# Performance work log

Hardware: AMD Instinct MI355X
Metric: run time of the kernel (lower is better)

Reference implementation:

```python
import jax, jax.numpy as jnp
import numpy as np
from jax import lax

WQ_MAX = 7.0    # int4 narrow symmetric range [-7, 7]
AQ_MAX = 15.0   # uint4 range [0, 15]
BN_EPS = 1e-5


def quant_weight(w):
    # per-output-channel symmetric int4 fake quant (OIHW, channel axis 0)
    s = jnp.max(jnp.abs(w), axis=(1, 2, 3), keepdims=True) / WQ_MAX
    s = jnp.maximum(s, 1e-8)
    return jnp.clip(jnp.round(w / s), -WQ_MAX, WQ_MAX) * s


def quant_relu(x, s):
    # ReLU fused with uint4 fake quant (clip at 0 subsumes ReLU)
    return jnp.clip(jnp.round(x / s), 0.0, AQ_MAX) * s


def conv2d(x, w, stride, pad, groups=1):
    return lax.conv_general_dilated(
        x, w, (stride, stride), [(pad, pad), (pad, pad)],
        feature_group_count=groups,
        dimension_numbers=('NCHW', 'OIHW', 'NCHW'))


def bn(x, g, b, m, v):
    inv = g / jnp.sqrt(v + BN_EPS)
    return x * inv[None, :, None, None] + (b - m * inv)[None, :, None, None]


def qconv_bn_qrelu(x, w, g, b, m, v, s, stride, pad, groups=1):
    x = conv2d(x, quant_weight(w), stride, pad, groups)
    return quant_relu(bn(x, g, b, m, v), s)


def setup_inputs() -> dict:
    key = jax.random.key(0)
    ks = jax.random.split(key, 8)
    d1, d2, oc = 32, 48, 64
    inp = {'x': jax.random.normal(ks[0], (8, 3, 512, 1024), dtype=jnp.float32)}

    def bn_params(c, tag):
        return {f'g{tag}': jnp.ones((c,), jnp.float32),
                f'b{tag}': jnp.zeros((c,), jnp.float32),
                f'm{tag}': jnp.zeros((c,), jnp.float32),
                f'v{tag}': jnp.ones((c,), jnp.float32)}

    inp['w1'] = 0.1 * jax.random.normal(ks[1], (d1, 3, 3, 3), jnp.float32)
    inp.update(bn_params(d1, 1)); inp['s1'] = jnp.float32(0.1)
    inp['wdw1'] = 0.1 * jax.random.normal(ks[2], (d1, 1, 3, 3), jnp.float32)
    inp.update(bn_params(d1, 2)); inp['s2'] = jnp.float32(0.1)
    inp['wpw1'] = 0.1 * jax.random.normal(ks[3], (d2, d1, 1, 1), jnp.float32)
    inp.update(bn_params(d2, 3)); inp['s3'] = jnp.float32(0.1)
    inp['wdw2'] = 0.1 * jax.random.normal(ks[4], (d2, 1, 3, 3), jnp.float32)
    inp.update(bn_params(d2, 4)); inp['s4'] = jnp.float32(0.1)
    inp['wpw2'] = 0.1 * jax.random.normal(ks[5], (oc, d2, 1, 1), jnp.float32)
    inp.update(bn_params(oc, 5)); inp['s5'] = jnp.float32(0.1)
    return inp


def reference(x, w1, g1, b1, m1, v1, s1,
              wdw1, g2, b2, m2, v2, s2,
              wpw1, g3, b3, m3, v3, s3,
              wdw2, g4, b4, m4, v4, s4,
              wpw2, g5, b5, m5, v5, s5):
    # _ConvBNReLU: 3x3 stride 2, padding 0
    x = qconv_bn_qrelu(x, w1, g1, b1, m1, v1, s1, stride=2, pad=0)
    # _DSConv 1: depthwise 3x3 s2 p1 (groups=32) + pointwise 1x1
    x = qconv_bn_qrelu(x, wdw1, g2, b2, m2, v2, s2, stride=2, pad=1, groups=32)
    x = qconv_bn_qrelu(x, wpw1, g3, b3, m3, v3, s3, stride=1, pad=0)
    # _DSConv 2: depthwise 3x3 s2 p1 (groups=48) + pointwise 1x1
    x = qconv_bn_qrelu(x, wdw2, g4, b4, m4, v4, s4, stride=2, pad=1, groups=48)
    x = qconv_bn_qrelu(x, wpw2, g5, b5, m5, v5, s5, stride=1, pad=0)
    return x  # [8, 64, 64, 128]
```

## Files before the change

kernel.cpp:

```cpp
#include <hip/hip_runtime.h>
#include <stdint.h>

#define AQ_MAX 15.0f
#define BN_EPS 1e-5f

__global__ __launch_bounds__(64) void prep_all(
    const float* __restrict__ wA, const float* __restrict__ gA,
    const float* __restrict__ bA, const float* __restrict__ mA,
    const float* __restrict__ vA,
    const float* __restrict__ wB, const float* __restrict__ gB,
    const float* __restrict__ bB, const float* __restrict__ mB,
    const float* __restrict__ vB,
    const float* __restrict__ wC, const float* __restrict__ gC,
    const float* __restrict__ bC, const float* __restrict__ mC,
    const float* __restrict__ vC,
    const float* __restrict__ wD, const float* __restrict__ gD,
    const float* __restrict__ bD, const float* __restrict__ mD,
    const float* __restrict__ vD,
    const float* __restrict__ wE, const float* __restrict__ gE,
    const float* __restrict__ bE, const float* __restrict__ mE,
    const float* __restrict__ vE,
    float* __restrict__ P) {
  int blk = blockIdx.x, t = threadIdx.x;
  const float *w, *g, *b, *m, *v;
  float *wq, *inv, *beta;
  int K, KP, c;
  if (blk < 32) {
    c = blk; w = wA; g = gA; b = bA; m = mA; v = vA; K = 27; KP = 28;
    wq = P + 0; inv = P + 6224; beta = P + 6256;
  } else if (blk < 64) {
    c = blk - 32; w = wB; g = gB; b = bB; m = mB; v = vB; K = 9; KP = 9;
    wq = P + 896; inv = P + 6288; beta = P + 6320;
  } else if (blk < 112) {
    c = blk - 64; w = wC; g = gC; b = bC; m = mC; v = vC; K = 32; KP = 32;
    wq = P + 1184; inv = P + 6352; beta = P + 6400;
  } else if (blk < 160) {
    c = blk - 112; w = wD; g = gD; b = bD; m = mD; v = vD; K = 9; KP = 9;
    wq = P + 2720; inv = P + 6448; beta = P + 6496;
  } else {
    c = blk - 160; w = wE; g = gE; b = bE; m = mE; v = vE; K = 48; KP = 48;
    wq = P + 3152; inv = P + 6544; beta = P + 6608;
  }
  const float* wc = w + (size_t)c * K;
  float a = (t < K) ? fabsf(wc[t]) : 0.0f;
#pragma unroll
  for (int off = 32; off >= 1; off >>= 1) a = fmaxf(a, __shfl_xor(a, off));
  float s = fmaxf(a / 7.0f, 1e-8f);
  if (t < K) {
    float q = rintf(wc[t] / s);
    q = fminf(7.0f, fmaxf(-7.0f, q));
    wq[(size_t)c * KP + t] = q * s;
  } else if (t < KP) {
    wq[(size_t)c * KP + t] = 0.0f;
  }
  if (t == 0) {
    float iv = g[c] / sqrtf(v[c] + BN_EPS);
    inv[c] = iv;
    beta[c] = b[c] - m[c] * iv;
  }
}

__global__ __launch_bounds__(256) void stage1_kernel(
    const float* __restrict__ x, const float* __restrict__ P,
    const float* __restrict__ s1p, uint8_t* __restrict__ out) {
  int tid = blockIdx.x * 256 + threadIdx.x;
  int gx = tid & 255;
  int t2 = tid >> 8;
  int oy = t2 % 255;
  int n = t2 / 255;
  float s1 = *s1p;
  int ix0 = gx * 4, iy = 2 * oy;
  bool tailok = (ix0 + 4) < 1024;
  float r[9][5];
#pragma unroll
  for (int ic = 0; ic < 3; ic++)
#pragma unroll
    for (int kh = 0; kh < 3; kh++) {
      const float* bp = x + (((size_t)(n * 3 + ic)) * 512 + (iy + kh)) * 1024 + ix0;
      float4 f = *(const float4*)bp;
      int s = ic * 3 + kh;
      r[s][0] = f.x; r[s][1] = f.y; r[s][2] = f.z; r[s][3] = f.w;
      r[s][4] = tailok ? bp[4] : 0.0f;
    }
  size_t obase = (((size_t)n * 32) * 255 + oy) * 256 + gx;
#pragma unroll 2
  for (int oc = 0; oc < 32; oc++) {
    const float* wp = P + oc * 28;
    float w[27];
#pragma unroll
    for (int j = 0; j < 27; j++) w[j] = wp[j];
    float a0 = 0.0f, a1 = 0.0f;
#pragma unroll
    for (int s = 0; s < 9; s++) {
#pragma unroll
      for (int kw = 0; kw < 3; kw++) {
        float wv = w[s * 3 + kw];
        a0 = fmaf(r[s][0 + kw], wv, a0);
        a1 = fmaf(r[s][2 + kw], wv, a1);
      }
    }
    float iv = P[6224 + oc], bt = P[6256 + oc];
    float y0 = fmaf(a0, iv, bt), y1 = fmaf(a1, iv, bt);
    uint32_t q0 = (uint32_t)fminf(AQ_MAX, fmaxf(0.0f, rintf(y0 / s1)));
    uint32_t q1 = (uint32_t)fminf(AQ_MAX, fmaxf(0.0f, rintf(y1 / s1)));
    out[obase + (size_t)oc * (255 * 256)] = (uint8_t)(q0 | (q1 << 4));
  }
}

template <int C, int IH, int IWL, int IWP, int OH, int OW, bool NIB>
__global__ __launch_bounds__(256) void dw_kernel(
    const uint8_t* __restrict__ in, const float* __restrict__ wq,
    const float* __restrict__ inv, const float* __restrict__ beta,
    const float* __restrict__ sin_p, const float* __restrict__ sout_p,
    uint8_t* __restrict__ out) {
  constexpr int GX = OW / 4;
  constexpr bool HASPAD = NIB ? (IWL < 2 * IWP) : (IWL < IWP);
  int tid = blockIdx.x * 256 + threadIdx.x;
  int oxg = tid % GX;
  int t2 = tid / GX;
  int oy = t2 % OH;
  int t3 = t2 / OH;
  int c = __builtin_amdgcn_readfirstlane(t3 % C);
  int n = __builtin_amdgcn_readfirstlane(t3 / C);
  float s_in = *sin_p, s_out = *sout_p;
  const float* wc = wq + c * 9;
  float w[9];
#pragma unroll
  for (int j = 0; j < 9; j++) w[j] = wc[j];
  float iv = inv[c], bt = beta[c];
  int c0 = oxg * 8;
  const uint8_t* chan = in + ((size_t)(n * C + c)) * IH * IWP;
  float xr[3][9];
#pragma unroll
  for (int kh = 0; kh < 3; kh++) {
    int iy = 2 * oy + kh - 1;
    if (iy >= 0 && iy < IH) {
      const uint8_t* rp = chan + (size_t)iy * IWP;
      if (NIB) {
        uint32_t u = *(const uint32_t*)(rp + c0 / 2);
        xr[kh][0] = (oxg > 0) ? (float)((rp[c0 / 2 - 1] >> 4) & 15u) : 0.0f;
#pragma unroll
        for (int j = 0; j < 8; j++)
          xr[kh][1 + j] = (float)((u >> (4 * j)) & 15u);
      } else {
        uint2 u = *(const uint2*)(rp + c0);
        xr[kh][0] = (oxg > 0) ? (float)rp[c0 - 1] : 0.0f;
#pragma unroll
        for (int j = 0; j < 4; j++) xr[kh][1 + j] = (float)((u.x >> (8 * j)) & 255u);
#pragma unroll
        for (int j = 0; j < 4; j++) xr[kh][5 + j] = (float)((u.y >> (8 * j)) & 255u);
      }
      if (HASPAD && oxg == GX - 1) xr[kh][8] = 0.0f;
    } else {
#pragma unroll
      for (int j = 0; j < 9; j++) xr[kh][j] = 0.0f;
    }
  }
#pragma unroll
  for (int kh = 0; kh < 3; kh++)
#pragma unroll
    for (int j = 0; j < 9; j++) xr[kh][j] *= s_in;
  float acc[4] = {0, 0, 0, 0};
#pragma unroll
  for (int kh = 0; kh < 3; kh++)
#pragma unroll
    for (int kw = 0; kw < 3; kw++) {
      float wv = w[kh * 3 + kw];
#pragma unroll
      for (int p = 0; p < 4; p++) acc[p] = fmaf(xr[kh][2 * p + kw], wv, acc[p]);
    }
  uint32_t pack = 0;
#pragma unroll
  for (int p = 0; p < 4; p++) {
    float y = fmaf(acc[p], iv, bt);
    float q = fminf(AQ_MAX, fmaxf(0.0f, rintf(y / s_out)));
    pack |= ((uint32_t)q) << (8 * p);
  }
  *(uint32_t*)(out + ((size_t)(n * C + c) * OH + oy) * OW + c0 / 2) = pack;
}

template <int IC, int OC, int CHUNK, int HW, bool FINAL, bool ROT>
__global__ __launch_bounds__(256) void pw_kernel(
    const uint8_t* __restrict__ in, const float* __restrict__ Pw,
    const float* __restrict__ Pinv, const float* __restrict__ Pbeta,
    const float* __restrict__ sin_p, const float* __restrict__ sout_p,
    void* __restrict__ outv) {
  constexpr int NCH = OC / CHUNK;
  int tid = blockIdx.x * 256 + threadIdx.x;
  int px = tid % HW;
  int rest = tid / HW;
  int chunk = __builtin_amdgcn_readfirstlane(rest % NCH);
  int n = __builtin_amdgcn_readfirstlane(rest / NCH);
  float s_in = *sin_p, s_out = *sout_p;
  const uint8_t* ib = in + (size_t)n * IC * HW + px;
  float xa[IC];
#pragma unroll
  for (int ic = 0; ic < IC; ic++)
    xa[ic] = (float)ib[(size_t)ic * HW] * s_in;
  int oc0 = chunk * CHUNK;
  if (ROT) {
    float wcur[IC], wnxt[IC], ivc, btc, ivn, btn;
#pragma unroll
    for (int j = 0; j < IC; j++) wcur[j] = Pw[(size_t)oc0 * IC + j];
    ivc = Pinv[oc0]; btc = Pbeta[oc0];
#pragma unroll
    for (int k = 0; k < CHUNK; k++) {
      int oc = oc0 + k;
      if (k < CHUNK - 1) {
#pragma unroll
        for (int j = 0; j < IC; j++) wnxt[j] = Pw[(size_t)(oc + 1) * IC + j];
        ivn = Pinv[oc + 1]; btn = Pbeta[oc + 1];
      }
      float a0 = 0;
#pragma unroll
      for (int ic = 0; ic < IC; ic++) a0 = fmaf(xa[ic], wcur[ic], a0);
      float y0 = fmaf(a0, ivc, btc);
      float q0 = fminf(AQ_MAX, fmaxf(0.0f, rintf(y0 / s_out)));
      if (FINAL) {
        ((float*)outv)[((size_t)n * OC + oc) * HW + px] = q0 * s_out;
      } else {
        ((uint8_t*)outv)[((size_t)n * OC + oc) * HW + px] = (uint8_t)q0;
      }
      if (k < CHUNK - 1) {
#pragma unroll
        for (int j = 0; j < IC; j++) wcur[j] = wnxt[j];
        ivc = ivn; btc = btn;
      }
    }
  } else {
#pragma unroll 2
    for (int oc = oc0; oc < oc0 + CHUNK; oc++) {
      const float* wp = Pw + (size_t)oc * IC;
      float w[IC];
#pragma unroll
      for (int ic = 0; ic < IC; ic++) w[ic] = wp[ic];
      float a0 = 0;
#pragma unroll
      for (int ic = 0; ic < IC; ic++) a0 = fmaf(xa[ic], w[ic], a0);
      float iv = Pinv[oc], bt = Pbeta[oc];
      float y0 = fmaf(a0, iv, bt);
      float q0 = fminf(AQ_MAX, fmaxf(0.0f, rintf(y0 / s_out)));
      if (FINAL) {
        ((float*)outv)[((size_t)n * OC + oc) * HW + px] = q0 * s_out;
      } else {
        ((uint8_t*)outv)[((size_t)n * OC + oc) * HW + px] = (uint8_t)q0;
      }
    }
  }
}

extern "C" void kernel_launch(void* const* d_in, const int* in_sizes, int n_in,
                              void* d_out, int out_size, void* d_ws, size_t ws_size,
                              hipStream_t stream) {
  const float* x    = (const float*)d_in[0];
  const float* w1   = (const float*)d_in[1];
  const float* g1   = (const float*)d_in[2];
  const float* b1   = (const float*)d_in[3];
  const float* m1   = (const float*)d_in[4];
  const float* v1   = (const float*)d_in[5];
  const float* s1   = (const float*)d_in[6];
  const float* wdw1 = (const float*)d_in[7];
  const float* g2   = (const float*)d_in[8];
  const float* b2   = (const float*)d_in[9];
  const float* m2   = (const float*)d_in[10];
  const float* v2   = (const float*)d_in[11];
  const float* s2   = (const float*)d_in[12];
  const float* wpw1 = (const float*)d_in[13];
  const float* g3   = (const float*)d_in[14];
  const float* b3   = (const float*)d_in[15];
  const float* m3   = (const float*)d_in[16];
  const float* v3   = (const float*)d_in[17];
  const float* s3   = (const float*)d_in[18];
  const float* wdw2 = (const float*)d_in[19];
  const float* g4   = (const float*)d_in[20];
  const float* b4   = (const float*)d_in[21];
  const float* m4   = (const float*)d_in[22];
  const float* v4   = (const float*)d_in[23];
  const float* s4   = (const float*)d_in[24];
  const float* wpw2 = (const float*)d_in[25];
  const float* g5   = (const float*)d_in[26];
  const float* b5   = (const float*)d_in[27];
  const float* m5   = (const float*)d_in[28];
  const float* v5   = (const float*)d_in[29];
  const float* s5   = (const float*)d_in[30];

  float* P = (float*)d_ws;
  float* wq2  = P + 896;
  float* wq3  = P + 1184;
  float* wq4  = P + 2720;
  float* wq5  = P + 3152;
  float* inv2 = P + 6288, *beta2 = P + 6320;
  float* inv3 = P + 6352, *beta3 = P + 6400;
  float* inv4 = P + 6448, *beta4 = P + 6496;
  float* inv5 = P + 6544, *beta5 = P + 6608;

  uint8_t* ws8 = (uint8_t*)d_ws;
  uint8_t* x1 = ws8 + 32768;
  uint8_t* x2 = x1 + 16711680;
  uint8_t* x3 = x2 + 8388608;
  uint8_t* x4 = ws8 + 32768;

  prep_all<<<224, 64, 0, stream>>>(w1, g1, b1, m1, v1,
                                   wdw1, g2, b2, m2, v2,
                                   wpw1, g3, b3, m3, v3,
                                   wdw2, g4, b4, m4, v4,
                                   wpw2, g5, b5, m5, v5, P);

  stage1_kernel<<<2040, 256, 0, stream>>>(x, P, s1, x1);
  dw_kernel<32, 255, 511, 256, 128, 256, true>
      <<<8192, 256, 0, stream>>>(x1, wq2, inv2, beta2, s1, s2, x2);
  pw_kernel<32, 48, 48, 32768, false, true>
      <<<1024, 256, 0, stream>>>(x2, wq3, inv3, beta3, s2, s3, x3);
  dw_kernel<48, 128, 256, 256, 64, 128, false>
      <<<3072, 256, 0, stream>>>(x3, wq4, inv4, beta4, s3, s4, x4);
  pw_kernel<48, 64, 16, 8192, true, false>
      <<<1024, 256, 0, stream>>>(x4, wq5, inv5, beta5, s4, s5, (float*)d_out);
}
```

Before: 113.4 us.

## Fuse pointwise1, depthwise2 and pointwise2 into one tiled shared-memory kernel

Replaces the last three kernels (pw1, dw2, pw2) with a single kernel. Each block handles an 8x8 output tile: it computes the 17x17 pw1 halo region into LDS, then the depthwise stride-2 conv into LDS, then the final pointwise conv straight to global memory. This removes the global round trips of the x3 and x4 intermediates and two kernel launches. In exchange it recomputes the halo overlap of pw1, and the second pass of the halo load leaves most threads idle.

```diff
diff --git a/kernel.cpp b/kernel.cpp
--- a/kernel.cpp
+++ b/kernel.cpp
@@ -179,72 +179,116 @@
   *(uint32_t*)(out + ((size_t)(n * C + c) * OH + oy) * OW + c0 / 2) = pack;
 }
 
-template <int IC, int OC, int CHUNK, int HW, bool FINAL, bool ROT>
-__global__ __launch_bounds__(256) void pw_kernel(
-    const uint8_t* __restrict__ in, const float* __restrict__ Pw,
-    const float* __restrict__ Pinv, const float* __restrict__ Pbeta,
-    const float* __restrict__ sin_p, const float* __restrict__ sout_p,
-    void* __restrict__ outv) {
-  constexpr int NCH = OC / CHUNK;
-  int tid = blockIdx.x * 256 + threadIdx.x;
-  int px = tid % HW;
-  int rest = tid / HW;
-  int chunk = __builtin_amdgcn_readfirstlane(rest % NCH);
-  int n = __builtin_amdgcn_readfirstlane(rest / NCH);
-  float s_in = *sin_p, s_out = *sout_p;
-  const uint8_t* ib = in + (size_t)n * IC * HW + px;
-  float xa[IC];
-#pragma unroll
-  for (int ic = 0; ic < IC; ic++)
-    xa[ic] = (float)ib[(size_t)ic * HW] * s_in;
-  int oc0 = chunk * CHUNK;
-  if (ROT) {
-    float wcur[IC], wnxt[IC], ivc, btc, ivn, btn;
-#pragma unroll
-    for (int j = 0; j < IC; j++) wcur[j] = Pw[(size_t)oc0 * IC + j];
-    ivc = Pinv[oc0]; btc = Pbeta[oc0];
-#pragma unroll
-    for (int k = 0; k < CHUNK; k++) {
-      int oc = oc0 + k;
-      if (k < CHUNK - 1) {
-#pragma unroll
-        for (int j = 0; j < IC; j++) wnxt[j] = Pw[(size_t)(oc + 1) * IC + j];
-        ivn = Pinv[oc + 1]; btn = Pbeta[oc + 1];
+__global__ __launch_bounds__(256) void fuse_tail(
+    const uint8_t* __restrict__ x2,
+    const float* __restrict__ Wpw1, const float* __restrict__ Ipw1,
+    const float* __restrict__ Bpw1,
+    const float* __restrict__ Wdw2, const float* __restrict__ Idw2,
+    const float* __restrict__ Bdw2,
+    const float* __restrict__ Wpw2, const float* __restrict__ Ipw2,
+    const float* __restrict__ Bpw2,
+    const float* __restrict__ s2p, const float* __restrict__ s3p,
+    const float* __restrict__ s4p, const float* __restrict__ s5p,
+    float* __restrict__ out) {
+  __shared__ uint8_t mid3[48 * 17 * 20];
+  __shared__ uint8_t mid4[48 * 8 * 12];
+  int bid = blockIdx.x;
+  int tx = bid & 15;
+  int t2b = bid >> 4;
+  int ty = t2b & 7;
+  int n = t2b >> 3;
+  int y0 = ty * 8, x0 = tx * 8;
+  float s2 = *s2p, s3 = *s3p, s4 = *s4p, s5 = *s5p;
+
+  for (int k = 0; k < 2; k++) {
+    int t = threadIdx.x + k * 256;
+    if (t < 289) {
+      int lr = t / 17, lc = t % 17;
+      int gr = 2 * y0 - 1 + lr, gc = 2 * x0 - 1 + lc;
+      if (gr < 0 || gc < 0) {
+#pragma unroll 4
+        for (int ch = 0; ch < 48; ch++) mid3[ch * 340 + lr * 20 + lc] = 0;
+      } else {
+        const uint8_t* ib = x2 + (size_t)n * 32 * 32768 + (size_t)gr * 256 + gc;
+        float xa[32];
+#pragma unroll
+        for (int ic = 0; ic < 32; ic++)
+          xa[ic] = (float)ib[(size_t)ic * 32768] * s2;
+#pragma unroll 2
+        for (int oc = 0; oc < 48; oc++) {
+          const float* wp = Wpw1 + oc * 32;
+          float w[32];
+#pragma unroll
+          for (int ic = 0; ic < 32; ic++) w[ic] = wp[ic];
+          float a0 = 0;
+#pragma unroll
+          for (int ic = 0; ic < 32; ic++) a0 = fmaf(xa[ic], w[ic], a0);
+          float y = fmaf(a0, Ipw1[oc], Bpw1[oc]);
+          float q = fminf(AQ_MAX, fmaxf(0.0f, rintf(y / s3)));
+          mid3[oc * 340 + lr * 20 + lc] = (uint8_t)q;
+        }
       }
+    }
+  }
+  __syncthreads();
+
+  {
+    int chg = __builtin_amdgcn_readfirstlane(threadIdx.x >> 6);
+    int pxid = threadIdx.x & 63;
+    int ly = pxid >> 3, lx = pxid & 7;
+#pragma unroll 2
+    for (int i = 0; i < 12; i++) {
+      int ch = chg * 12 + i;
+      const float* wc = Wdw2 + ch * 9;
+      float w[9];
+#pragma unroll
+      for (int j = 0; j < 9; j++) w[j] = wc[j];
+      float iv = Idw2[ch], bt = Bdw2[ch];
+      float xr[3][3];
+#pragma unroll
+      for (int kh = 0; kh < 3; kh++)
+#pragma unroll
+        for (int kw = 0; kw < 3; kw++)
+          xr[kh][kw] = (float)mid3[ch * 340 + (2 * ly + kh) * 20 + (2 * lx + kw)];
+#pragma unroll
+      for (int kh = 0; kh < 3; kh++)
+#pragma unroll
+        for (int kw = 0; kw < 3; kw++) xr[kh][kw] *= s3;
+      float acc = 0;
+#pragma unroll
+      for (int kh = 0; kh < 3; kh++)
+#pragma unroll
+        for (int kw = 0; kw < 3; kw++)
+          acc = fmaf(xr[kh][kw], w[kh * 3 + kw], acc);
+      float y = fmaf(acc, iv, bt);
+      float q = fminf(AQ_MAX, fmaxf(0.0f, rintf(y / s4)));
+      mid4[ch * 96 + ly * 12 + lx] = (uint8_t)q;
+    }
+  }
+  __syncthreads();
+
+  {
+    int ocg = __builtin_amdgcn_readfirstlane(threadIdx.x >> 6);
+    int pxid = threadIdx.x & 63;
+    int ly = pxid >> 3, lx = pxid & 7;
+    float xa[48];
+#pragma unroll
+    for (int ic = 0; ic < 48; ic++)
+      xa[ic] = (float)mid4[ic * 96 + ly * 12 + lx] * s4;
+    size_t ob = ((size_t)n * 64) * (64 * 128) + (size_t)(y0 + ly) * 128 + (x0 + lx);
+#pragma unroll 2
+    for (int k = 0; k < 16; k++) {
+      int oc = ocg * 16 + k;
+      const float* wp = Wpw2 + oc * 48;
+      float w[48];
+#pragma unroll
+      for (int ic = 0; ic < 48; ic++) w[ic] = wp[ic];
       float a0 = 0;
 #pragma unroll
-      for (int ic = 0; ic < IC; ic++) a0 = fmaf(xa[ic], wcur[ic], a0);
-      float y0 = fmaf(a0, ivc, btc);
-      float q0 = fminf(AQ_MAX, fmaxf(0.0f, rintf(y0 / s_out)));
-      if (FINAL) {
-        ((float*)outv)[((size_t)n * OC + oc) * HW + px] = q0 * s_out;
-      } else {
-        ((uint8_t*)outv)[((size_t)n * OC + oc) * HW + px] = (uint8_t)q0;
-      }
-      if (k < CHUNK - 1) {
-#pragma unroll
-        for (int j = 0; j < IC; j++) wcur[j] = wnxt[j];
-        ivc = ivn; btc = btn;
-      }
-    }
-  } else {
-#pragma unroll 2
-    for (int oc = oc0; oc < oc0 + CHUNK; oc++) {
-      const float* wp = Pw + (size_t)oc * IC;
-      float w[IC];
-#pragma unroll
-      for (int ic = 0; ic < IC; ic++) w[ic] = wp[ic];
-      float a0 = 0;
-#pragma unroll
-      for (int ic = 0; ic < IC; ic++) a0 = fmaf(xa[ic], w[ic], a0);
-      float iv = Pinv[oc], bt = Pbeta[oc];
-      float y0 = fmaf(a0, iv, bt);
-      float q0 = fminf(AQ_MAX, fmaxf(0.0f, rintf(y0 / s_out)));
-      if (FINAL) {
-        ((float*)outv)[((size_t)n * OC + oc) * HW + px] = q0 * s_out;
-      } else {
-        ((uint8_t*)outv)[((size_t)n * OC + oc) * HW + px] = (uint8_t)q0;
-      }
+      for (int ic = 0; ic < 48; ic++) a0 = fmaf(xa[ic], w[ic], a0);
+      float y = fmaf(a0, Ipw2[oc], Bpw2[oc]);
+      float q = fminf(AQ_MAX, fmaxf(0.0f, rintf(y / s5)));
+      out[ob + (size_t)oc * (64 * 128)] = q * s5;
     }
   }
 }
@@ -297,8 +341,6 @@
   uint8_t* ws8 = (uint8_t*)d_ws;
   uint8_t* x1 = ws8 + 32768;
   uint8_t* x2 = x1 + 16711680;
-  uint8_t* x3 = x2 + 8388608;
-  uint8_t* x4 = ws8 + 32768;
 
   prep_all<<<224, 64, 0, stream>>>(w1, g1, b1, m1, v1,
                                    wdw1, g2, b2, m2, v2,
@@ -309,10 +351,8 @@
   stage1_kernel<<<2040, 256, 0, stream>>>(x, P, s1, x1);
   dw_kernel<32, 255, 511, 256, 128, 256, true>
       <<<8192, 256, 0, stream>>>(x1, wq2, inv2, beta2, s1, s2, x2);
-  pw_kernel<32, 48, 48, 32768, false, true>
-      <<<1024, 256, 0, stream>>>(x2, wq3, inv3, beta3, s2, s3, x3);
-  dw_kernel<48, 128, 256, 256, 64, 128, false>
-      <<<3072, 256, 0, stream>>>(x3, wq4, inv4, beta4, s3, s4, x4);
-  pw_kernel<48, 64, 16, 8192, true, false>
-      <<<1024, 256, 0, stream>>>(x4, wq5, inv5, beta5, s4, s5, (float*)d_out);
-}
+  fuse_tail<<<1024, 256, 0, stream>>>(x2, wq3, inv3, beta3,
+                                      wq4, inv4, beta4,
+                                      wq5, inv5, beta5,
+                                      s2, s3, s4, s5, (float*)d_out);
+}
```

After: 128.9 us. +13.7%, slower.
